# Kernel optimization log

Hardware: AMD Instinct MI355X
Metric: run time of the kernel (lower is better)

## Reference

```python
import jax, jax.numpy as jnp
import numpy as np
from jax.scipy.special import erf

N_POINTS = 4096
N_EVENTS = 1000000
BETA = 1.0   # init_beta, constant (not a Parameter in the torch module)
ALPHA = 1.0  # torch.ones((1,1)) buffer
WEIGHT = 1.0


def setup_inputs() -> dict:
    key = jax.random.key(0)
    k1, k2, k3, k4, k5 = jax.random.split(key, 5)
    return {
        "z0": jax.random.uniform(k1, (N_POINTS, 2), dtype=jnp.float32),
        "v0": jax.random.uniform(k2, (N_POINTS, 2), dtype=jnp.float32),
        "event_times": jax.random.uniform(k3, (N_EVENTS,), dtype=jnp.float32),
        "t0": jnp.zeros((), dtype=jnp.float32),
        "tn": jnp.ones((), dtype=jnp.float32),
        "u_idx": jax.random.randint(k4, (N_EVENTS,), 0, N_POINTS, dtype=jnp.int64) if jax.config.read('jax_enable_x64') else jax.random.randint(k4, (N_EVENTS,), 0, N_POINTS).astype(jnp.int32),
        "v_idx": jax.random.randint(k5, (N_EVENTS,), 0, N_POINTS).astype(jnp.int32),
    }


def reference(z0, v0, event_times, t0, tn, u_idx, v_idx):
    beta = jnp.float32(BETA)
    alpha = jnp.float32(ALPHA)

    # ---- event term: sum_e beta - ||z_u(t_e) - z_v(t_e)||^2,  z(t) = z0 + v0*t (a0 == 0)
    dz0 = z0[u_idx] - z0[v_idx]                      # [E, 2]
    dv0 = v0[u_idx] - v0[v_idx]                      # [E, 2]
    dz = dz0 + dv0 * event_times[:, None]            # [E, 2]
    d2 = jnp.sum(dz * dz, axis=-1)                   # [E]
    event_intensity = jnp.sum(beta - d2)

    # ---- non-event term: analytic Hawkes integral over all triu pairs
    i, j = jnp.triu_indices(z0.shape[0], k=1)        # static, [P]
    a = z0[i, 0] - z0[j, 0]
    b = z0[i, 1] - z0[j, 1]
    m = v0[i, 0] - v0[j, 0]
    n = v0[i, 1] - v0[j, 1]
    mn2 = m * m + n * n                              # [P]
    s = jnp.sqrt(alpha * mn2)
    cross = a * n - b * m
    dot = a * m + b * n
    expo = jnp.exp((-(cross * cross) * alpha + mn2 * beta) / mn2)
    sqrt_pi = jnp.float32(np.sqrt(np.pi))
    integral = (-sqrt_pi * expo
                * (erf(alpha * (mn2 * t0 + dot) / s) - erf(alpha * (mn2 * tn + dot) / s))
                / (2.0 * s))                          # [P]
    non_event_intensity = jnp.sum(integral)

    return event_intensity - WEIGHT * non_event_intensity
```

## Files before the change

kernel.cpp:

```cpp
#include <hip/hip_runtime.h>

typedef float v2f __attribute__((ext_vector_type(2)));
typedef unsigned int v2u __attribute__((ext_vector_type(2)));

#define NPTS   4096
#define NEVT   1000000
#define NQUAD  (NEVT / 4)
#define TILE   64
#define NT     (NPTS / TILE)
#define PAIR_BLOCKS (NT * (NT + 1) / 2)
#define BLK    512
#define GRID   512
#define NWAVES (GRID * (BLK / 64))
#define NUNITS (PAIR_BLOCKS * 4)
#define PERW   (NUNITS / NWAVES)
#define REMW   (NUNITS % NWAVES)

#define LOG2E  1.4426950408889634f
#define EA1 0.278393f
#define EA2 0.230389f
#define EA3 0.000972f
#define EA4 0.078108f

__device__ __forceinline__ v2f vabs2(v2f x) {
    return (v2f){__builtin_fabsf(x.x), __builtin_fabsf(x.y)};
}
__device__ __forceinline__ v2f signed_one_minus(v2f q, v2f s) {
    v2f r = (v2f){1.0f, 1.0f} - q;
    v2u ru, su;
    __builtin_memcpy(&ru, &r, 8);
    __builtin_memcpy(&su, &s, 8);
    ru |= (su & (v2u){0x80000000u, 0x80000000u});
    v2f o;
    __builtin_memcpy(&o, &ru, 8);
    return o;
}

__global__ __launch_bounds__(BLK, 4) void hawkes_fused(
    const float* __restrict__ z0, const float* __restrict__ v0,
    const float* __restrict__ et, const float* __restrict__ t0p,
    const float* __restrict__ tnp, const int* __restrict__ uix,
    const int* __restrict__ vix, float* __restrict__ out)
{
    __shared__ float sx[NPTS], sy[NPTS], sz[NPTS], sw[NPTS];
    __shared__ float red[BLK / 64];
    const int tid = threadIdx.x;

    const float t0 = *t0p;
    const float tn = *tnp;

    {
        const float4* z4 = (const float4*)z0;
        const float4* vv4 = (const float4*)v0;
        #pragma unroll
        for (int k = 0; k < NPTS / (2 * BLK); ++k) {
            int p2 = tid + k * BLK;
            float4 zz = z4[p2];
            float4 vv = vv4[p2];
            sx[2 * p2] = zz.x; sx[2 * p2 + 1] = zz.z;
            sy[2 * p2] = zz.y; sy[2 * p2 + 1] = zz.w;
            sz[2 * p2] = vv.x; sz[2 * p2 + 1] = vv.z;
            sw[2 * p2] = vv.y; sw[2 * p2 + 1] = vv.w;
        }
    }
    __syncthreads();

    float acc_ev = 0.0f;
    {
        int q = (int)blockIdx.x * BLK + tid;
        if (q < NQUAD) {
            int base = q * 4;
            float4 t4 = *(const float4*)(et + base);
            int4   u4 = *(const int4*)(uix + base);
            int4   v4 = *(const int4*)(vix + base);
            float tt[4] = {t4.x, t4.y, t4.z, t4.w};
            int   uu[4] = {u4.x, u4.y, u4.z, u4.w};
            int   vv[4] = {v4.x, v4.y, v4.z, v4.w};
            #pragma unroll
            for (int e = 0; e < 4; ++e) {
                int a = uu[e], b = vv[e];
                float dx = __builtin_fmaf(sz[a] - sz[b], tt[e], sx[a] - sx[b]);
                float dy = __builtin_fmaf(sw[a] - sw[b], tt[e], sy[a] - sy[b]);
                acc_ev += 1.0f - (dx * dx + dy * dy);
            }
        }
    }

    const v2f t0v = (v2f){t0, t0};
    const v2f tnv = (v2f){tn, tn};
    const v2f l2e = (v2f){LOG2E, LOG2E};
    const int il  = tid & 63;
    const int wid = (int)blockIdx.x * (BLK / 64) + (tid >> 6);
    int un   = wid * PERW + (wid < REMW ? wid : REMW);
    int nend = un + PERW + (wid < REMW ? 1 : 0);
    v2f accp = (v2f){0.0f, 0.0f};
    for (; un < nend; ++un) {
        int L    = un >> 2;
        int quad = un & 3;
        int bi = (int)((129.0f - sqrtf((float)(16641 - 8 * L))) * 0.5f);
        while (bi * NT - bi * (bi - 1) / 2 > L) --bi;
        while ((bi + 1) * NT - (bi + 1) * bi / 2 <= L) ++bi;
        int bj = bi + (L - (bi * NT - bi * (bi - 1) / 2));
        int ibase = bi * TILE;
        int jb    = bj * TILE + (quad << 4);
        int i = ibase + il;
        v2f pix = (v2f){sx[i], sx[i]};
        v2f piy = (v2f){sy[i], sy[i]};
        v2f piz = (v2f){sz[i], sz[i]};
        v2f piw = (v2f){sw[i], sw[i]};
        #pragma unroll
        for (int k = 0; k < 8; ++k) {
            int j0 = jb + (k << 1);
            v2f tjx = *(const v2f*)&sx[j0];
            v2f tjy = *(const v2f*)&sy[j0];
            v2f tjz = *(const v2f*)&sz[j0];
            v2f tjw = *(const v2f*)&sw[j0];
            v2f a  = pix - tjx;
            v2f b  = piy - tjy;
            v2f m  = piz - tjz;
            v2f n  = piw - tjw;
            v2f mn2 = m * m + n * n;
            v2f cr  = a * n - b * m;
            v2f dt  = a * m + b * n;
            v2f invs = (v2f){__builtin_amdgcn_rsqf(mn2.x),
                             __builtin_amdgcn_rsqf(mn2.y)};
            v2f g   = cr * cr * (invs * invs);
            v2f exv = l2e - g * l2e;
            v2f ee  = (v2f){__builtin_amdgcn_exp2f(exv.x),
                            __builtin_amdgcn_exp2f(exv.y)};
            v2f A   = (mn2 * t0v + dt) * invs;
            v2f B   = (mn2 * tnv + dt) * invs;
            v2f xA  = vabs2(A), xB = vabs2(B);
            v2f PA  = (v2f){1.0f,1.0f} + xA*((v2f){EA1,EA1} + xA*((v2f){EA2,EA2}
                        + xA*((v2f){EA3,EA3} + xA*(v2f){EA4,EA4})));
            v2f PB  = (v2f){1.0f,1.0f} + xB*((v2f){EA1,EA1} + xB*((v2f){EA2,EA2}
                        + xB*((v2f){EA3,EA3} + xB*(v2f){EA4,EA4})));
            v2f PP  = PA * PB;
            v2f R   = (v2f){__builtin_amdgcn_rcpf(PP.x),
                            __builtin_amdgcn_rcpf(PP.y)};
            v2f rA  = R * PB, rB = R * PA;
            v2f qA  = rA * rA; qA *= qA;
            v2f qB  = rB * rB; qB *= qB;
            v2f eA  = signed_one_minus(qA, A);
            v2f eB  = signed_one_minus(qB, B);
            v2f term = (eB - eA) * ee * invs;
            v2f sel = (v2f){ (j0     > i) ? term.x : 0.0f,
                             (j0 + 1 > i) ? term.y : 0.0f };
            accp += sel;
        }
    }

    float contrib = __builtin_fmaf(-0.8862269254527580f, accp.x + accp.y, acc_ev);

    #pragma unroll
    for (int off = 32; off > 0; off >>= 1)
        contrib += __shfl_down(contrib, off, 64);
    if ((tid & 63) == 0) red[tid >> 6] = contrib;
    __syncthreads();
    if (tid == 0) {
        float s = 0.0f;
        #pragma unroll
        for (int w = 0; w < BLK / 64; ++w) s += red[w];
        atomicAdd(out, s);
    }
}

extern "C" void kernel_launch(void* const* d_in, const int* in_sizes, int n_in,
                              void* d_out, int out_size, void* d_ws, size_t ws_size,
                              hipStream_t stream) {
    const float* z0  = (const float*)d_in[0];
    const float* v0  = (const float*)d_in[1];
    const float* et  = (const float*)d_in[2];
    const float* t0p = (const float*)d_in[3];
    const float* tnp = (const float*)d_in[4];
    const int*   uix = (const int*)d_in[5];
    const int*   vix = (const int*)d_in[6];
    float* out = (float*)d_out;

    hipLaunchKernelGGL(hawkes_fused, dim3(GRID), dim3(BLK), 0, stream,
                       z0, v0, et, t0p, tnp, uix, vix, out);
}
```

Measured before the change: 82.86 us.

## Pack points as float4 in LDS, read j-columns via scalar global loads, split diagonal tiles

Replaces the four separate LDS arrays with one float4-per-point array, so each event gather and each i-point load becomes a single 128-bit LDS read. In the pair loop the j-column values, which are uniform across the wave, are read straight from global memory, so the compiler can use scalar loads instead of LDS broadcasts. The triangular mask is applied only on diagonal tiles through a templated helper, and the per-wave work split is hardcoded with readfirstlane. The hardcoded split depends on the exact unit count, and the unroll drops from 8 to 4.

```diff
diff --git a/kernel.cpp b/kernel.cpp
--- a/kernel.cpp
+++ b/kernel.cpp
@@ -1,7 +1,6 @@
 #include <hip/hip_runtime.h>
 
 typedef float v2f __attribute__((ext_vector_type(2)));
-typedef unsigned int v2u __attribute__((ext_vector_type(2)));
 
 #define NPTS   4096
 #define NEVT   1000000
@@ -13,8 +12,6 @@
 #define GRID   512
 #define NWAVES (GRID * (BLK / 64))
 #define NUNITS (PAIR_BLOCKS * 4)
-#define PERW   (NUNITS / NWAVES)
-#define REMW   (NUNITS % NWAVES)
 
 #define LOG2E  1.4426950408889634f
 #define EA1 0.278393f
@@ -25,15 +22,49 @@
 __device__ __forceinline__ v2f vabs2(v2f x) {
     return (v2f){__builtin_fabsf(x.x), __builtin_fabsf(x.y)};
 }
-__device__ __forceinline__ v2f signed_one_minus(v2f q, v2f s) {
-    v2f r = (v2f){1.0f, 1.0f} - q;
-    v2u ru, su;
-    __builtin_memcpy(&ru, &r, 8);
-    __builtin_memcpy(&su, &s, 8);
-    ru |= (su & (v2u){0x80000000u, 0x80000000u});
-    v2f o;
-    __builtin_memcpy(&o, &ru, 8);
-    return o;
+
+template<bool DIAG>
+__device__ __forceinline__ v2f col2(v2f pix, v2f piy, v2f piz, v2f piw,
+                                    v2f tjx, v2f tjy, v2f tjz, v2f tjw,
+                                    v2f t0v, v2f tnv, v2f l2e,
+                                    int j0, int i)
+{
+    v2f a  = pix - tjx;
+    v2f b  = piy - tjy;
+    v2f m  = piz - tjz;
+    v2f n  = piw - tjw;
+    v2f mn2 = m * m + n * n;
+    v2f cr  = a * n - b * m;
+    v2f dt  = a * m + b * n;
+    v2f invs = (v2f){__builtin_amdgcn_rsqf(mn2.x),
+                     __builtin_amdgcn_rsqf(mn2.y)};
+    v2f g   = cr * cr * (invs * invs);
+    v2f exv = l2e - g * l2e;
+    v2f ee  = (v2f){__builtin_amdgcn_exp2f(exv.x),
+                    __builtin_amdgcn_exp2f(exv.y)};
+    v2f A   = (mn2 * t0v + dt) * invs;
+    v2f B   = (mn2 * tnv + dt) * invs;
+    v2f xA  = vabs2(A), xB = vabs2(B);
+    v2f PA  = (v2f){1.0f,1.0f} + xA*((v2f){EA1,EA1} + xA*((v2f){EA2,EA2}
+                + xA*((v2f){EA3,EA3} + xA*(v2f){EA4,EA4})));
+    v2f PB  = (v2f){1.0f,1.0f} + xB*((v2f){EA1,EA1} + xB*((v2f){EA2,EA2}
+                + xB*((v2f){EA3,EA3} + xB*(v2f){EA4,EA4})));
+    v2f PP  = PA * PB;
+    v2f R   = (v2f){__builtin_amdgcn_rcpf(PP.x),
+                    __builtin_amdgcn_rcpf(PP.y)};
+    v2f rA  = R * PB, rB = R * PA;
+    v2f qA  = rA * rA; qA *= qA;
+    v2f qB  = rB * rB; qB *= qB;
+    v2f eA  = (v2f){__builtin_copysignf(1.0f - qA.x, A.x),
+                    __builtin_copysignf(1.0f - qA.y, A.y)};
+    v2f eB  = (v2f){__builtin_copysignf(1.0f - qB.x, B.x),
+                    __builtin_copysignf(1.0f - qB.y, B.y)};
+    v2f term = (eB - eA) * ee * invs;
+    if (DIAG) {
+        term.x = (j0     > i) ? term.x : 0.0f;
+        term.y = (j0 + 1 > i) ? term.y : 0.0f;
+    }
+    return term;
 }
 
 __global__ __launch_bounds__(BLK, 4) void hawkes_fused(
@@ -42,7 +73,7 @@
     const float* __restrict__ tnp, const int* __restrict__ uix,
     const int* __restrict__ vix, float* __restrict__ out)
 {
-    __shared__ float sx[NPTS], sy[NPTS], sz[NPTS], sw[NPTS];
+    __shared__ float4 sp[NPTS];
     __shared__ float red[BLK / 64];
     const int tid = threadIdx.x;
 
@@ -51,16 +82,14 @@
 
     {
         const float4* z4 = (const float4*)z0;
-        const float4* vv4 = (const float4*)v0;
+        const float4* w4 = (const float4*)v0;
         #pragma unroll
         for (int k = 0; k < NPTS / (2 * BLK); ++k) {
             int p2 = tid + k * BLK;
             float4 zz = z4[p2];
-            float4 vv = vv4[p2];
-            sx[2 * p2] = zz.x; sx[2 * p2 + 1] = zz.z;
-            sy[2 * p2] = zz.y; sy[2 * p2 + 1] = zz.w;
-            sz[2 * p2] = vv.x; sz[2 * p2 + 1] = vv.z;
-            sw[2 * p2] = vv.y; sw[2 * p2 + 1] = vv.w;
+            float4 vv = w4[p2];
+            sp[2 * p2]     = (float4){zz.x, zz.y, vv.x, vv.y};
+            sp[2 * p2 + 1] = (float4){zz.z, zz.w, vv.z, vv.w};
         }
     }
     __syncthreads();
@@ -78,9 +107,10 @@
             int   vv[4] = {v4.x, v4.y, v4.z, v4.w};
             #pragma unroll
             for (int e = 0; e < 4; ++e) {
-                int a = uu[e], b = vv[e];
-                float dx = __builtin_fmaf(sz[a] - sz[b], tt[e], sx[a] - sx[b]);
-                float dy = __builtin_fmaf(sw[a] - sw[b], tt[e], sy[a] - sy[b]);
+                float4 pa = sp[uu[e]];
+                float4 pb = sp[vv[e]];
+                float dx = __builtin_fmaf(pa.z - pb.z, tt[e], pa.x - pb.x);
+                float dy = __builtin_fmaf(pa.w - pb.w, tt[e], pa.y - pb.y);
                 acc_ev += 1.0f - (dx * dx + dy * dy);
             }
         }
@@ -90,63 +120,47 @@
     const v2f tnv = (v2f){tn, tn};
     const v2f l2e = (v2f){LOG2E, LOG2E};
     const int il  = tid & 63;
-    const int wid = (int)blockIdx.x * (BLK / 64) + (tid >> 6);
-    int un   = wid * PERW + (wid < REMW ? wid : REMW);
-    int nend = un + PERW + (wid < REMW ? 1 : 0);
+    const int wid = __builtin_amdgcn_readfirstlane(
+                        (int)blockIdx.x * (BLK / 64) + (tid >> 6));
+    int un  = 2 * wid + ((wid + 31) >> 5);
+    int cnt = 2 + ((wid & 31) == 0 ? 1 : 0);
     v2f accp = (v2f){0.0f, 0.0f};
-    for (; un < nend; ++un) {
+    for (int it = 0; it < cnt; ++it, ++un) {
         int L    = un >> 2;
         int quad = un & 3;
         int bi = (int)((129.0f - sqrtf((float)(16641 - 8 * L))) * 0.5f);
         while (bi * NT - bi * (bi - 1) / 2 > L) --bi;
         while ((bi + 1) * NT - (bi + 1) * bi / 2 <= L) ++bi;
         int bj = bi + (L - (bi * NT - bi * (bi - 1) / 2));
-        int ibase = bi * TILE;
-        int jb    = bj * TILE + (quad << 4);
-        int i = ibase + il;
-        v2f pix = (v2f){sx[i], sx[i]};
-        v2f piy = (v2f){sy[i], sy[i]};
-        v2f piz = (v2f){sz[i], sz[i]};
-        v2f piw = (v2f){sw[i], sw[i]};
-        #pragma unroll
-        for (int k = 0; k < 8; ++k) {
-            int j0 = jb + (k << 1);
-            v2f tjx = *(const v2f*)&sx[j0];
-            v2f tjy = *(const v2f*)&sy[j0];
-            v2f tjz = *(const v2f*)&sz[j0];
-            v2f tjw = *(const v2f*)&sw[j0];
-            v2f a  = pix - tjx;
-            v2f b  = piy - tjy;
-            v2f m  = piz - tjz;
-            v2f n  = piw - tjw;
-            v2f mn2 = m * m + n * n;
-            v2f cr  = a * n - b * m;
-            v2f dt  = a * m + b * n;
-            v2f invs = (v2f){__builtin_amdgcn_rsqf(mn2.x),
-                             __builtin_amdgcn_rsqf(mn2.y)};
-            v2f g   = cr * cr * (invs * invs);
-            v2f exv = l2e - g * l2e;
-            v2f ee  = (v2f){__builtin_amdgcn_exp2f(exv.x),
-                            __builtin_amdgcn_exp2f(exv.y)};
-            v2f A   = (mn2 * t0v + dt) * invs;
-            v2f B   = (mn2 * tnv + dt) * invs;
-            v2f xA  = vabs2(A), xB = vabs2(B);
-            v2f PA  = (v2f){1.0f,1.0f} + xA*((v2f){EA1,EA1} + xA*((v2f){EA2,EA2}
-                        + xA*((v2f){EA3,EA3} + xA*(v2f){EA4,EA4})));
-            v2f PB  = (v2f){1.0f,1.0f} + xB*((v2f){EA1,EA1} + xB*((v2f){EA2,EA2}
-                        + xB*((v2f){EA3,EA3} + xB*(v2f){EA4,EA4})));
-            v2f PP  = PA * PB;
-            v2f R   = (v2f){__builtin_amdgcn_rcpf(PP.x),
-                            __builtin_amdgcn_rcpf(PP.y)};
-            v2f rA  = R * PB, rB = R * PA;
-            v2f qA  = rA * rA; qA *= qA;
-            v2f qB  = rB * rB; qB *= qB;
-            v2f eA  = signed_one_minus(qA, A);
-            v2f eB  = signed_one_minus(qB, B);
-            v2f term = (eB - eA) * ee * invs;
-            v2f sel = (v2f){ (j0     > i) ? term.x : 0.0f,
-                             (j0 + 1 > i) ? term.y : 0.0f };
-            accp += sel;
+        int jc = bj * TILE + (quad << 4);
+        int i  = bi * TILE + il;
+        float4 pi4 = sp[i];
+        v2f pix = (v2f){pi4.x, pi4.x};
+        v2f piy = (v2f){pi4.y, pi4.y};
+        v2f piz = (v2f){pi4.z, pi4.z};
+        v2f piw = (v2f){pi4.w, pi4.w};
+        const float* zj = z0 + 2 * jc;
+        const float* vj = v0 + 2 * jc;
+        if (bi != bj) {
+            #pragma unroll 4
+            for (int k = 0; k < 8; ++k) {
+                v2f tjx = (v2f){zj[4 * k],     zj[4 * k + 2]};
+                v2f tjy = (v2f){zj[4 * k + 1], zj[4 * k + 3]};
+                v2f tjz = (v2f){vj[4 * k],     vj[4 * k + 2]};
+                v2f tjw = (v2f){vj[4 * k + 1], vj[4 * k + 3]};
+                accp += col2<false>(pix, piy, piz, piw, tjx, tjy, tjz, tjw,
+                                    t0v, tnv, l2e, 0, 0);
+            }
+        } else {
+            #pragma unroll 4
+            for (int k = 0; k < 8; ++k) {
+                v2f tjx = (v2f){zj[4 * k],     zj[4 * k + 2]};
+                v2f tjy = (v2f){zj[4 * k + 1], zj[4 * k + 3]};
+                v2f tjz = (v2f){vj[4 * k],     vj[4 * k + 2]};
+                v2f tjw = (v2f){vj[4 * k + 1], vj[4 * k + 3]};
+                accp += col2<true>(pix, piy, piz, piw, tjx, tjy, tjz, tjw,
+                                   t0v, tnv, l2e, jc + 2 * k, i);
+            }
         }
     }
 
```

After: 82.08 us. About the same (-0.9%).
